# Performance work log

Hardware: AMD Instinct MI355X
Metric: run time of the kernel (lower is better)

The kernel has to match this reference:

```python
import jax, jax.numpy as jnp
import numpy as np

N = 50000      # nodes
E = 800000     # edges (before self-loops)
F_IN = 128     # num_features
HID = 32       # hidden_channels
HEADS = 4
CLS = 40       # num_classes
NEG_SLOPE = 0.2


def setup_inputs() -> dict:
    key = jax.random.key(0)
    ks = jax.random.split(key, 10)
    s = 0.1
    x = jax.random.normal(ks[0], (N, F_IN), jnp.float32)
    edge_index = jax.random.randint(ks[1], (2, E), 0, N, jnp.int32)
    W1 = jax.random.normal(ks[2], (F_IN, HEADS * HID), jnp.float32) * s
    att_src1 = jax.random.normal(ks[3], (HEADS, HID), jnp.float32) * s
    att_dst1 = jax.random.normal(ks[4], (HEADS, HID), jnp.float32) * s
    b1 = jnp.zeros((HEADS * HID,), jnp.float32)
    W2 = jax.random.normal(ks[5], (HEADS * HID, CLS), jnp.float32) * s
    att_src2 = jax.random.normal(ks[6], (1, CLS), jnp.float32) * s
    att_dst2 = jax.random.normal(ks[7], (1, CLS), jnp.float32) * s
    b2 = jnp.zeros((CLS,), jnp.float32)
    return {"x": x, "edge_index": edge_index,
            "W1": W1, "att_src1": att_src1, "att_dst1": att_dst1, "b1": b1,
            "W2": W2, "att_src2": att_src2, "att_dst2": att_dst2, "b2": b2}


def gat_layer(x, src, dst, W, a_src, a_dst, b, concat):
    """PyG GATConv: per-head linear, edge attention logits a_src.h_j + a_dst.h_i,
    LeakyReLU, segment softmax over incoming edges per dst, weighted scatter-sum."""
    n = x.shape[0]
    H, C = a_src.shape
    h = (x @ W).reshape(n, H, C)                       # [N, H, C]
    al_s = jnp.einsum('nhc,hc->nh', h, a_src)          # [N, H]
    al_d = jnp.einsum('nhc,hc->nh', h, a_dst)          # [N, H]
    e = jax.nn.leaky_relu(al_s[src] + al_d[dst], NEG_SLOPE)  # [E, H]
    e_max = jax.lax.stop_gradient(jax.ops.segment_max(e, dst, num_segments=n))
    e = jnp.exp(e - e_max[dst])
    denom = jax.ops.segment_sum(e, dst, num_segments=n)      # [N, H]
    alpha = e / (denom[dst] + 1e-16)                         # [E, H]
    out = jax.ops.segment_sum(h[src] * alpha[:, :, None], dst, num_segments=n)  # [N, H, C]
    out = out.reshape(n, H * C) if concat else out.mean(axis=1)
    return out + b


def reference(x, edge_index, W1, att_src1, att_dst1, b1, W2, att_src2, att_dst2, b2):
    n = x.shape[0]
    loops = jnp.arange(n, dtype=edge_index.dtype)
    src = jnp.concatenate([edge_index[0], loops])  # PyG adds self-loops by default
    dst = jnp.concatenate([edge_index[1], loops])
    h = gat_layer(x, src, dst, W1, att_src1, att_dst1, b1, concat=True)
    h = jax.nn.relu(h)  # dropout is identity in eval mode
    h = gat_layer(h, src, dst, W2, att_src2, att_dst2, b2, concat=False)
    return jax.nn.log_softmax(h, axis=1)
```

## Files before the change

kernel.cpp:

```cpp
#include <hip/hip_runtime.h>
#include <hip/hip_bf16.h>
#include <cstdint>
#include <cstddef>

#define NN 50000
#define EE 800000
#define ETOT (EE + NN)
#define FIN 128
#define D1 128
#define HEADS 4
#define HID 32
#define CLS 40
#define NEG 0.2f
#define MAXDEG 64
#define NPART 8
#define PSIZE 6250
#define GB 104
#define BGB (NPART * GB)

typedef __attribute__((ext_vector_type(8))) short short8;
typedef __attribute__((ext_vector_type(4))) float float4v;

union U16 { uint4 u; short8 s; };

__device__ __forceinline__ float bf2f(unsigned short u) {
    union { unsigned int i; float f; } v; v.i = ((unsigned int)u) << 16; return v.f;
}
__device__ __forceinline__ unsigned short f2bf(float f) {
    union { unsigned int i; float f; } v; v.f = f;
    unsigned int r = v.i + 0x7fffu + ((v.i >> 16) & 1u);
    return (unsigned short)(r >> 16);
}

__global__ __launch_bounds__(256) void bg_k(const int* __restrict__ eidx,
                                            int* __restrict__ cnt,
                                            unsigned short* __restrict__ ssrcp,
                                            const float* __restrict__ X,
                                            const float* __restrict__ W,
                                            const float* __restrict__ as1,
                                            const float* __restrict__ ad1,
                                            unsigned int* __restrict__ H1b,
                                            float* __restrict__ ALS1,
                                            float* __restrict__ ALD1) {
    __shared__ uint4 Wl[2048];
    __shared__ float sas[128], sad[128];
    int t = threadIdx.x;

    if (blockIdx.x < BGB) {
        int part = blockIdx.x & (NPART - 1);
        int g    = blockIdx.x >> 3;
        int lo = part * PSIZE, hi = lo + PSIZE;
        int stride = GB * 256;
        for (int i = g * 256 + t; i < ETOT; i += stride) {
            int dN = (i < EE) ? eidx[EE + i] : (i - EE);
            if (dN >= lo && dN < hi) {
                int sN = (i < EE) ? eidx[i] : dN;
                int slot = atomicAdd(&cnt[dN], 1);
                if (slot < MAXDEG) ssrcp[dN * MAXDEG + slot] = (unsigned short)sN;
            }
        }
        return;
    }

    int bI = blockIdx.x - BGB;
    if (t < 128) { sas[t] = as1[t]; sad[t] = ad1[t]; }
    for (int g = t; g < 2048; g += 256) {
        int ct = g >> 8, rem = g & 255, kc = rem >> 6, l = rem & 63;
        int c = ct * 16 + (l & 15);
        int k0 = kc * 32 + (l >> 4) * 8;
        U16 u;
#pragma unroll
        for (int j = 0; j < 8; j++) u.s[j] = (short)f2bf(W[(k0 + j) * D1 + c]);
        Wl[g] = u.u;
    }
    __syncthreads();

    int wid = t >> 6, lane = t & 63, quad = lane >> 4, lrow = lane & 15;
    int wrow0 = bI * 128 + wid * 32;

    short8 afr[2][4];
#pragma unroll
    for (int rt = 0; rt < 2; rt++) {
        int r = wrow0 + rt * 16 + lrow;
#pragma unroll
        for (int kc = 0; kc < 4; kc++) {
            short8 a = {0, 0, 0, 0, 0, 0, 0, 0};
            if (r < NN) {
                const float* xp = X + (size_t)r * FIN + kc * 32 + quad * 8;
                float4 x0 = *(const float4*)xp;
                float4 x1 = *(const float4*)(xp + 4);
                a[0] = (short)f2bf(x0.x); a[1] = (short)f2bf(x0.y);
                a[2] = (short)f2bf(x0.z); a[3] = (short)f2bf(x0.w);
                a[4] = (short)f2bf(x1.x); a[5] = (short)f2bf(x1.y);
                a[6] = (short)f2bf(x1.z); a[7] = (short)f2bf(x1.w);
            }
            afr[rt][kc] = a;
        }
    }

    float4v acc[2][8];
#pragma unroll
    for (int rt = 0; rt < 2; rt++)
#pragma unroll
        for (int ct = 0; ct < 8; ct++) acc[rt][ct] = (float4v)(0.f);

#pragma unroll
    for (int ct = 0; ct < 8; ct++) {
#pragma unroll
        for (int kc = 0; kc < 4; kc++) {
            U16 b; b.u = Wl[(ct * 4 + kc) * 64 + lane];
            acc[0][ct] = __builtin_amdgcn_mfma_f32_16x16x32_bf16(afr[0][kc], b.s, acc[0][ct], 0, 0, 0);
            acc[1][ct] = __builtin_amdgcn_mfma_f32_16x16x32_bf16(afr[1][kc], b.s, acc[1][ct], 0, 0, 0);
        }
    }

#pragma unroll
    for (int rt = 0; rt < 2; rt++) {
#pragma unroll
        for (int reg = 0; reg < 4; reg++) {
            float ps[4] = {0.f, 0.f, 0.f, 0.f};
            float pd[4] = {0.f, 0.f, 0.f, 0.f};
#pragma unroll
            for (int ct = 0; ct < 8; ct++) {
                float v = acc[rt][ct][reg];
                ps[ct >> 1] += v * sas[ct * 16 + lrow];
                pd[ct >> 1] += v * sad[ct * 16 + lrow];
            }
#pragma unroll
            for (int o = 1; o < 16; o <<= 1) {
#pragma unroll
                for (int h = 0; h < 4; h++) {
                    ps[h] += __shfl_xor(ps[h], o);
                    pd[h] += __shfl_xor(pd[h], o);
                }
            }
            int r = wrow0 + rt * 16 + quad * 4 + reg;
            if (lrow == 0 && r < NN) {
                *(float4*)&ALS1[(size_t)r * 4] = make_float4(ps[0], ps[1], ps[2], ps[3]);
                *(float4*)&ALD1[(size_t)r * 4] = make_float4(pd[0], pd[1], pd[2], pd[3]);
            }
        }
    }

#pragma unroll
    for (int rt = 0; rt < 2; rt++)
#pragma unroll
        for (int ct = 0; ct < 8; ct++)
#pragma unroll
            for (int reg = 0; reg < 4; reg++) {
                float v = acc[rt][ct][reg];
                float o = __shfl_xor(v, 1);
                int r = wrow0 + rt * 16 + quad * 4 + reg;
                if (((lane & 1) == 0) && r < NN) {
                    unsigned int u = (unsigned int)f2bf(v) | ((unsigned int)f2bf(o) << 16);
                    H1b[(size_t)r * 64 + ct * 8 + (lrow >> 1)] = u;
                }
            }
}

__global__ __launch_bounds__(256) void gather1_k(const int* __restrict__ cnt,
                                                 const unsigned short* __restrict__ ssrcp,
                                                 const uint4* __restrict__ H1b4,
                                                 const float4* __restrict__ ALS,
                                                 const float4* __restrict__ ALD,
                                                 const float* __restrict__ b1,
                                                 uint4* __restrict__ OUT1b4) {
    __shared__ float wlds[4][MAXDEG][4];
    __shared__ int sidlds[4][MAXDEG];
    int wid = threadIdx.x >> 6, lane = threadIdx.x & 63;
    int v = blockIdx.x * 4 + wid;
    int deg = min(cnt[v], MAXDEG);
    float4 ad = ALD[v];
    float w0 = 0.f, w1 = 0.f, w2 = 0.f, w3 = 0.f;
    if (lane < deg) {
        int s = (int)ssrcp[v * MAXDEG + lane];
        sidlds[wid][lane] = s;
        float4 as = ALS[s];
        float l0 = as.x + ad.x; l0 = l0 > 0.f ? l0 : NEG * l0;
        float l1 = as.y + ad.y; l1 = l1 > 0.f ? l1 : NEG * l1;
        float l2 = as.z + ad.z; l2 = l2 > 0.f ? l2 : NEG * l2;
        float l3 = as.w + ad.w; l3 = l3 > 0.f ? l3 : NEG * l3;
        w0 = __expf(l0); w1 = __expf(l1); w2 = __expf(l2); w3 = __expf(l3);
        wlds[wid][lane][0] = w0; wlds[wid][lane][1] = w1;
        wlds[wid][lane][2] = w2; wlds[wid][lane][3] = w3;
    }
    float d0 = w0, d1 = w1, d2 = w2, d3 = w3;
#pragma unroll
    for (int o = 1; o < 64; o <<= 1) {
        d0 += __shfl_xor(d0, o); d1 += __shfl_xor(d1, o);
        d2 += __shfl_xor(d2, o); d3 += __shfl_xor(d3, o);
    }
    __syncthreads();
    int g = lane >> 4, l = lane & 15, head = l >> 2;
    float a0=0.f,a1=0.f,a2=0.f,a3=0.f,a4=0.f,a5=0.f,a6=0.f,a7=0.f;
    for (int j = g; j < deg; j += 4) {
        float wj = wlds[wid][j][head];
        int s = sidlds[wid][j];
        uint4 q = H1b4[(size_t)s * 16 + l];
        a0 += wj * bf2f((unsigned short)(q.x & 0xffffu));
        a1 += wj * bf2f((unsigned short)(q.x >> 16));
        a2 += wj * bf2f((unsigned short)(q.y & 0xffffu));
        a3 += wj * bf2f((unsigned short)(q.y >> 16));
        a4 += wj * bf2f((unsigned short)(q.z & 0xffffu));
        a5 += wj * bf2f((unsigned short)(q.z >> 16));
        a6 += wj * bf2f((unsigned short)(q.w & 0xffffu));
        a7 += wj * bf2f((unsigned short)(q.w >> 16));
    }
#pragma unroll
    for (int o = 16; o < 64; o <<= 1) {
        a0 += __shfl_xor(a0, o); a1 += __shfl_xor(a1, o);
        a2 += __shfl_xor(a2, o); a3 += __shfl_xor(a3, o);
        a4 += __shfl_xor(a4, o); a5 += __shfl_xor(a5, o);
        a6 += __shfl_xor(a6, o); a7 += __shfl_xor(a7, o);
    }
    if (lane < 16) {
        float den = (head == 0) ? d0 : (head == 1) ? d1 : (head == 2) ? d2 : d3;
        den += 1e-16f;
        float4 bA = *(const float4*)&b1[8 * l];
        float4 bB = *(const float4*)&b1[8 * l + 4];
        float o0 = fmaxf(a0 / den + bA.x, 0.f);
        float o1 = fmaxf(a1 / den + bA.y, 0.f);
        float o2 = fmaxf(a2 / den + bA.z, 0.f);
        float o3 = fmaxf(a3 / den + bA.w, 0.f);
        float o4 = fmaxf(a4 / den + bB.x, 0.f);
        float o5 = fmaxf(a5 / den + bB.y, 0.f);
        float o6 = fmaxf(a6 / den + bB.z, 0.f);
        float o7 = fmaxf(a7 / den + bB.w, 0.f);
        uint4 u;
        u.x = (unsigned int)f2bf(o0) | ((unsigned int)f2bf(o1) << 16);
        u.y = (unsigned int)f2bf(o2) | ((unsigned int)f2bf(o3) << 16);
        u.z = (unsigned int)f2bf(o4) | ((unsigned int)f2bf(o5) << 16);
        u.w = (unsigned int)f2bf(o6) | ((unsigned int)f2bf(o7) << 16);
        OUT1b4[(size_t)v * 16 + l] = u;
    }
}

__global__ __launch_bounds__(256) void gemm2_k(const unsigned int* __restrict__ OUT1b,
                                               const float* __restrict__ W2,
                                               const float* __restrict__ as2,
                                               const float* __restrict__ ad2,
                                               unsigned int* __restrict__ H2b,
                                               float* __restrict__ ALS2,
                                               float* __restrict__ ALD2) {
    __shared__ uint4 Wl[768];
    __shared__ float sas[48], sad[48];
    int t = threadIdx.x;
    if (t < 48) {
        sas[t] = (t < CLS) ? as2[t] : 0.f;
        sad[t] = (t < CLS) ? ad2[t] : 0.f;
    }
    for (int g = t; g < 768; g += 256) {
        int ct = g >> 8, rem = g & 255, kc = rem >> 6, l = rem & 63;
        int c = ct * 16 + (l & 15);
        int k0 = kc * 32 + (l >> 4) * 8;
        U16 u;
#pragma unroll
        for (int j = 0; j < 8; j++)
            u.s[j] = (c < CLS) ? (short)f2bf(W2[(k0 + j) * CLS + c]) : (short)0;
        Wl[g] = u.u;
    }
    __syncthreads();

    int wid = t >> 6, lane = t & 63, quad = lane >> 4, lrow = lane & 15;
    int wrow0 = blockIdx.x * 128 + wid * 32;

    U16 afr[2][4];
#pragma unroll
    for (int rt = 0; rt < 2; rt++) {
        int r = wrow0 + rt * 16 + lrow;
#pragma unroll
        for (int kc = 0; kc < 4; kc++) {
            if (r < NN)
                afr[rt][kc].u = ((const uint4*)OUT1b)[(size_t)r * 16 + kc * 4 + quad];
            else
                afr[rt][kc].u = make_uint4(0, 0, 0, 0);
        }
    }

    float4v acc[2][3];
#pragma unroll
    for (int rt = 0; rt < 2; rt++)
#pragma unroll
        for (int ct = 0; ct < 3; ct++) acc[rt][ct] = (float4v)(0.f);

#pragma unroll
    for (int ct = 0; ct < 3; ct++) {
#pragma unroll
        for (int kc = 0; kc < 4; kc++) {
            U16 b; b.u = Wl[(ct * 4 + kc) * 64 + lane];
            acc[0][ct] = __builtin_amdgcn_mfma_f32_16x16x32_bf16(afr[0][kc].s, b.s, acc[0][ct], 0, 0, 0);
            acc[1][ct] = __builtin_amdgcn_mfma_f32_16x16x32_bf16(afr[1][kc].s, b.s, acc[1][ct], 0, 0, 0);
        }
    }

#pragma unroll
    for (int rt = 0; rt < 2; rt++) {
#pragma unroll
        for (int reg = 0; reg < 4; reg++) {
            float ps = 0.f, pd = 0.f;
#pragma unroll
            for (int ct = 0; ct < 3; ct++) {
                float v = acc[rt][ct][reg];
                ps += v * sas[ct * 16 + lrow];
                pd += v * sad[ct * 16 + lrow];
            }
#pragma unroll
            for (int o = 1; o < 16; o <<= 1) {
                ps += __shfl_xor(ps, o);
                pd += __shfl_xor(pd, o);
            }
            int r = wrow0 + rt * 16 + quad * 4 + reg;
            if (lrow == 0 && r < NN) {
                ALS2[r] = ps;
                ALD2[r] = pd;
            }
        }
    }

#pragma unroll
    for (int rt = 0; rt < 2; rt++)
#pragma unroll
        for (int ct = 0; ct < 3; ct++)
#pragma unroll
            for (int reg = 0; reg < 4; reg++) {
                float v = acc[rt][ct][reg];
                float o = __shfl_xor(v, 1);
                int r = wrow0 + rt * 16 + quad * 4 + reg;
                int c = ct * 16 + lrow;
                if (((lane & 1) == 0) && c < CLS && r < NN) {
                    unsigned int u = (unsigned int)f2bf(v) | ((unsigned int)f2bf(o) << 16);
                    H2b[(size_t)r * 20 + (c >> 1)] = u;
                }
            }
}

__global__ __launch_bounds__(64) void gather2_k(const int* __restrict__ cnt,
                                                const unsigned short* __restrict__ ssrcp,
                                                const unsigned int* __restrict__ H2b,
                                                const float* __restrict__ ALS,
                                                const float* __restrict__ ALD,
                                                const float* __restrict__ b2,
                                                float* __restrict__ out) {
    int v = blockIdx.x, t = threadIdx.x;
    int deg = min(cnt[v], MAXDEG);
    __shared__ float w[MAXDEG];
    __shared__ int sid[MAXDEG];
    __shared__ float part[2][CLS];
    float den = 0.f;
    float adv = ALD[v];
    if (t < deg) {
        int s = (int)ssrcp[v * MAXDEG + t];
        sid[t] = s;
        float l = ALS[s] + adv; l = l > 0.f ? l : NEG * l;
        float e = __expf(l);
        w[t] = e; den = e;
    }
    __syncthreads();
    int g = t >> 5, c = t & 31;
    if (c < 20) {
        float ax = 0.f, ay = 0.f;
        for (int j = g; j < deg; j += 2) {
            float wj = w[j];
            unsigned int u = H2b[(size_t)sid[j] * 20 + c];
            ax += wj * bf2f((unsigned short)(u & 0xffffu));
            ay += wj * bf2f((unsigned short)(u >> 16));
        }
        part[g][2 * c] = ax;
        part[g][2 * c + 1] = ay;
    }
#pragma unroll
    for (int o = 32; o > 0; o >>= 1) den += __shfl_xor(den, o);
    __syncthreads();
    float z = (t < CLS) ? (part[0][t] + part[1][t]) / (den + 1e-16f) + b2[t] : -1e30f;
    float mx = z;
#pragma unroll
    for (int o = 32; o > 0; o >>= 1) mx = fmaxf(mx, __shfl_xor(mx, o));
    float ex = (t < CLS) ? __expf(z - mx) : 0.f;
    float se = ex;
#pragma unroll
    for (int o = 32; o > 0; o >>= 1) se += __shfl_xor(se, o);
    if (t < CLS) out[(size_t)v * CLS + t] = z - mx - __logf(se);
}

extern "C" void kernel_launch(void* const* d_in, const int* in_sizes, int n_in,
                              void* d_out, int out_size, void* d_ws, size_t ws_size,
                              hipStream_t stream) {
    const float* x   = (const float*)d_in[0];
    const int*   eix = (const int*)d_in[1];
    const float* W1  = (const float*)d_in[2];
    const float* as1 = (const float*)d_in[3];
    const float* ad1 = (const float*)d_in[4];
    const float* b1  = (const float*)d_in[5];
    const float* W2  = (const float*)d_in[6];
    const float* as2 = (const float*)d_in[7];
    const float* ad2 = (const float*)d_in[8];
    const float* b2  = (const float*)d_in[9];
    float* out = (float*)d_out;

    char* p = (char*)d_ws;
    auto carve = [&](size_t bytes) -> void* {
        void* r = (void*)p;
        p += (bytes + 255) & ~(size_t)255;
        return r;
    };
    unsigned int* H1b   = (unsigned int*)carve((size_t)NN * 64 * 4);
    unsigned int* OUT1b = (unsigned int*)carve((size_t)NN * 64 * 4);
    unsigned int* H2b   = (unsigned int*)carve((size_t)NN * 20 * 4);
    float* ALS1 = (float*)carve((size_t)NN * 4 * 4);
    float* ALD1 = (float*)carve((size_t)NN * 4 * 4);
    float* ALS2 = (float*)carve((size_t)NN * 4);
    float* ALD2 = (float*)carve((size_t)NN * 4);
    int* cnt    = (int*)carve((size_t)NN * 4);
    unsigned short* ssrcp = (unsigned short*)carve((size_t)NN * MAXDEG * 2);

    hipMemsetAsync(cnt, 0, (size_t)NN * 4, stream);

    int gemmBlocks = (NN + 127) / 128;
    bg_k<<<BGB + gemmBlocks, 256, 0, stream>>>(eix, cnt, ssrcp, x, W1, as1, ad1,
                                               H1b, ALS1, ALD1);
    gather1_k<<<NN / 4, 256, 0, stream>>>(cnt, ssrcp, (const uint4*)H1b,
                                          (const float4*)ALS1, (const float4*)ALD1,
                                          b1, (uint4*)OUT1b);
    gemm2_k<<<(NN + 127) / 128, 256, 0, stream>>>(OUT1b, W2, as2, ad2, H2b, ALS2, ALD2);
    gather2_k<<<NN, 64, 0, stream>>>(cnt, ssrcp, H2b, ALS2, ALD2, b2, out);
}
```

Measured before the change: 232.1 us.

## Use nontemporal loads/stores for streamed buffers and pack four nodes per gather2 block

```diff
diff --git a/kernel.cpp b/kernel.cpp
--- a/kernel.cpp
+++ b/kernel.cpp
@@ -20,8 +20,10 @@
 
 typedef __attribute__((ext_vector_type(8))) short short8;
 typedef __attribute__((ext_vector_type(4))) float float4v;
-
-union U16 { uint4 u; short8 s; };
+typedef __attribute__((ext_vector_type(4))) float floatx4;
+typedef __attribute__((ext_vector_type(4))) unsigned int uintx4;
+
+union U16 { uint4 u; uintx4 x; short8 s; };
 
 __device__ __forceinline__ float bf2f(unsigned short u) {
     union { unsigned int i; float f; } v; v.i = ((unsigned int)u) << 16; return v.f;
@@ -52,9 +54,9 @@
         int lo = part * PSIZE, hi = lo + PSIZE;
         int stride = GB * 256;
         for (int i = g * 256 + t; i < ETOT; i += stride) {
-            int dN = (i < EE) ? eidx[EE + i] : (i - EE);
+            int dN = (i < EE) ? __builtin_nontemporal_load(&eidx[EE + i]) : (i - EE);
             if (dN >= lo && dN < hi) {
-                int sN = (i < EE) ? eidx[i] : dN;
+                int sN = (i < EE) ? __builtin_nontemporal_load(&eidx[i]) : dN;
                 int slot = atomicAdd(&cnt[dN], 1);
                 if (slot < MAXDEG) ssrcp[dN * MAXDEG + slot] = (unsigned short)sN;
             }
@@ -87,8 +89,8 @@
             short8 a = {0, 0, 0, 0, 0, 0, 0, 0};
             if (r < NN) {
                 const float* xp = X + (size_t)r * FIN + kc * 32 + quad * 8;
-                float4 x0 = *(const float4*)xp;
-                float4 x1 = *(const float4*)(xp + 4);
+                floatx4 x0 = __builtin_nontemporal_load((const floatx4*)xp);
+                floatx4 x1 = __builtin_nontemporal_load((const floatx4*)(xp + 4));
                 a[0] = (short)f2bf(x0.x); a[1] = (short)f2bf(x0.y);
                 a[2] = (short)f2bf(x0.z); a[3] = (short)f2bf(x0.w);
                 a[4] = (short)f2bf(x1.x); a[5] = (short)f2bf(x1.y);
@@ -153,7 +155,7 @@
                 int r = wrow0 + rt * 16 + quad * 4 + reg;
                 if (((lane & 1) == 0) && r < NN) {
                     unsigned int u = (unsigned int)f2bf(v) | ((unsigned int)f2bf(o) << 16);
-                    H1b[(size_t)r * 64 + ct * 8 + (lrow >> 1)] = u;
+                    __builtin_nontemporal_store(u, &H1b[(size_t)r * 64 + ct * 8 + (lrow >> 1)]);
                 }
             }
 }
@@ -164,7 +166,7 @@
                                                  const float4* __restrict__ ALS,
                                                  const float4* __restrict__ ALD,
                                                  const float* __restrict__ b1,
-                                                 uint4* __restrict__ OUT1b4) {
+                                                 unsigned int* __restrict__ OUT1b) {
     __shared__ float wlds[4][MAXDEG][4];
     __shared__ int sidlds[4][MAXDEG];
     int wid = threadIdx.x >> 6, lane = threadIdx.x & 63;
@@ -226,12 +228,12 @@
         float o5 = fmaxf(a5 / den + bB.y, 0.f);
         float o6 = fmaxf(a6 / den + bB.z, 0.f);
         float o7 = fmaxf(a7 / den + bB.w, 0.f);
-        uint4 u;
+        uintx4 u;
         u.x = (unsigned int)f2bf(o0) | ((unsigned int)f2bf(o1) << 16);
         u.y = (unsigned int)f2bf(o2) | ((unsigned int)f2bf(o3) << 16);
         u.z = (unsigned int)f2bf(o4) | ((unsigned int)f2bf(o5) << 16);
         u.w = (unsigned int)f2bf(o6) | ((unsigned int)f2bf(o7) << 16);
-        OUT1b4[(size_t)v * 16 + l] = u;
+        __builtin_nontemporal_store(u, (uintx4*)&OUT1b[(size_t)v * 64 + l * 4]);
     }
 }
 
@@ -271,9 +273,10 @@
 #pragma unroll
         for (int kc = 0; kc < 4; kc++) {
             if (r < NN)
-                afr[rt][kc].u = ((const uint4*)OUT1b)[(size_t)r * 16 + kc * 4 + quad];
+                afr[rt][kc].x = __builtin_nontemporal_load(
+                    (const uintx4*)&OUT1b[(size_t)r * 64 + (kc * 4 + quad) * 4]);
             else
-                afr[rt][kc].u = make_uint4(0, 0, 0, 0);
+                afr[rt][kc].x = (uintx4)(0u);
         }
     }
 
@@ -334,52 +337,58 @@
             }
 }
 
-__global__ __launch_bounds__(64) void gather2_k(const int* __restrict__ cnt,
-                                                const unsigned short* __restrict__ ssrcp,
-                                                const unsigned int* __restrict__ H2b,
-                                                const float* __restrict__ ALS,
-                                                const float* __restrict__ ALD,
-                                                const float* __restrict__ b2,
-                                                float* __restrict__ out) {
-    int v = blockIdx.x, t = threadIdx.x;
+__global__ __launch_bounds__(256) void gather2_k(const int* __restrict__ cnt,
+                                                 const unsigned short* __restrict__ ssrcp,
+                                                 const unsigned int* __restrict__ H2b,
+                                                 const float* __restrict__ ALS,
+                                                 const float* __restrict__ ALD,
+                                                 const float* __restrict__ b2,
+                                                 float* __restrict__ out) {
+    __shared__ float wlds[4][MAXDEG];
+    __shared__ int sidlds[4][MAXDEG];
+    int wid = threadIdx.x >> 6, lane = threadIdx.x & 63;
+    int v = blockIdx.x * 4 + wid;
     int deg = min(cnt[v], MAXDEG);
-    __shared__ float w[MAXDEG];
-    __shared__ int sid[MAXDEG];
-    __shared__ float part[2][CLS];
-    float den = 0.f;
     float adv = ALD[v];
-    if (t < deg) {
-        int s = (int)ssrcp[v * MAXDEG + t];
-        sid[t] = s;
+    float e = 0.f;
+    if (lane < deg) {
+        int s = (int)ssrcp[v * MAXDEG + lane];
+        sidlds[wid][lane] = s;
         float l = ALS[s] + adv; l = l > 0.f ? l : NEG * l;
-        float e = __expf(l);
-        w[t] = e; den = e;
-    }
-    __syncthreads();
-    int g = t >> 5, c = t & 31;
+        e = __expf(l);
+        wlds[wid][lane] = e;
+    }
+    float den = e;
+#pragma unroll
+    for (int o = 1; o < 64; o <<= 1) den += __shfl_xor(den, o);
+    den += 1e-16f;
+    int g = lane >> 5, c = lane & 31;
+    float ax = 0.f, ay = 0.f;
     if (c < 20) {
-        float ax = 0.f, ay = 0.f;
         for (int j = g; j < deg; j += 2) {
-            float wj = w[j];
-            unsigned int u = H2b[(size_t)sid[j] * 20 + c];
+            float wj = wlds[wid][j];
+            unsigned int u = H2b[(size_t)sidlds[wid][j] * 20 + c];
             ax += wj * bf2f((unsigned short)(u & 0xffffu));
             ay += wj * bf2f((unsigned short)(u >> 16));
         }
-        part[g][2 * c] = ax;
-        part[g][2 * c + 1] = ay;
-    }
-#pragma unroll
-    for (int o = 32; o > 0; o >>= 1) den += __shfl_xor(den, o);
-    __syncthreads();
-    float z = (t < CLS) ? (part[0][t] + part[1][t]) / (den + 1e-16f) + b2[t] : -1e30f;
-    float mx = z;
-#pragma unroll
-    for (int o = 32; o > 0; o >>= 1) mx = fmaxf(mx, __shfl_xor(mx, o));
-    float ex = (t < CLS) ? __expf(z - mx) : 0.f;
-    float se = ex;
-#pragma unroll
-    for (int o = 32; o > 0; o >>= 1) se += __shfl_xor(se, o);
-    if (t < CLS) out[(size_t)v * CLS + t] = z - mx - __logf(se);
+    }
+    ax += __shfl_xor(ax, 32);
+    ay += __shfl_xor(ay, 32);
+    float z0 = -1e30f, z1 = -1e30f;
+    if (c < 20) {
+        z0 = ax / den + b2[2 * c];
+        z1 = ay / den + b2[2 * c + 1];
+    }
+    float m = fmaxf(z0, z1);
+#pragma unroll
+    for (int o = 1; o < 32; o <<= 1) m = fmaxf(m, __shfl_xor(m, o));
+    float se = (c < 20) ? (__expf(z0 - m) + __expf(z1 - m)) : 0.f;
+#pragma unroll
+    for (int o = 1; o < 32; o <<= 1) se += __shfl_xor(se, o);
+    float ls = __logf(se);
+    if (g == 0 && c < 20) {
+        *(float2*)&out[(size_t)v * CLS + 2 * c] = make_float2(z0 - m - ls, z1 - m - ls);
+    }
 }
 
 extern "C" void kernel_launch(void* const* d_in, const int* in_sizes, int n_in,
@@ -420,7 +429,7 @@
                                                H1b, ALS1, ALD1);
     gather1_k<<<NN / 4, 256, 0, stream>>>(cnt, ssrcp, (const uint4*)H1b,
                                           (const float4*)ALS1, (const float4*)ALD1,
-                                          b1, (uint4*)OUT1b);
+                                          b1, OUT1b);
     gemm2_k<<<(NN + 127) / 128, 256, 0, stream>>>(OUT1b, W2, as2, ad2, H2b, ALS2, ALD2);
-    gather2_k<<<NN, 64, 0, stream>>>(cnt, ssrcp, H2b, ALS2, ALD2, b2, out);
-}
+    gather2_k<<<NN / 4, 256, 0, stream>>>(cnt, ssrcp, H2b, ALS2, ALD2, b2, out);
+}
```

Result: slower. 257.4 us (+10.9%).
